# Optimization experiments

Hardware: AMD Instinct MI355X
Metric: run time of the kernel (lower is better)

## Reference

```python
import jax, jax.numpy as jnp
import numpy as np

PI = np.pi
B_IN, B1, B2 = 30, 10, 6      # bandwidths: input S2, after conv1, after conv2
F1, F2, F_OUT = 20, 40, 10


def _wigner_d_stack(l, betas):
    """Wigner-d d^l_{mn}(beta) = <m|exp(-i beta Jy)|n> (real), shape [nbeta, 2l+1, 2l+1]."""
    n = 2 * l + 1
    m = np.arange(-l, l)
    c = np.sqrt(l * (l + 1) - m * (m + 1))          # J+ couplings m -> m+1
    Jp = np.zeros((n, n))
    Jp[np.arange(1, n), np.arange(n - 1)] = c
    A = 0.5 * (Jp.T - Jp)                            # exp(beta*A) = d^l(beta)
    ev, V = np.linalg.eig(A)
    Vi = np.linalg.inv(V)
    E = np.exp(np.multiply.outer(np.asarray(betas, np.float64), ev))
    return np.einsum('mk,bk,kn->bmn', V, E, Vi).real


def _qw(b):
    """Driscoll-Healy quadrature weights over beta for the SOFT grid of bandwidth b."""
    j = np.arange(2 * b)
    theta = PI * (2 * j + 1) / (4 * b)
    k = np.arange(b)
    return (2.0 / b) * np.sin(theta) * (np.sin(theta[:, None] * (2 * k + 1)) / (2 * k + 1)).sum(1)


def _betas(b):
    return PI * (2 * np.arange(2 * b) + 1) / (4 * b)


def _s2_grid():   # s2_near_identity_grid(): 3 betas x 8 alphas = 24 points
    beta = np.arange(1, 4) * (PI / 8) / 3
    alpha = np.linspace(0, 2 * PI, 8, endpoint=False)
    B, A = np.meshgrid(beta, alpha, indexing='ij')
    return B.ravel(), A.ravel()


def _so3_grid():  # so3_near_identity_grid(): 3x8x8 = 192 points, gamma = pre_gamma - alpha
    beta = np.arange(1, 4) * (PI / 8) / 3
    alpha = np.linspace(0, 2 * PI, 8, endpoint=False)
    pre_gamma = np.linspace(-2 * PI, 2 * PI, 8, endpoint=False)
    B, A, C = np.meshgrid(beta, alpha, pre_gamma, indexing='ij')
    return B.ravel(), A.ravel(), (C - A).ravel()


# ---------- static spectral constants (numpy, built once at import) ----------
_bet_in, _w_in = _betas(B_IN), _qw(B_IN)
_bet1, _w1 = _betas(B1), _qw(B1)
_bet2, _w2 = _betas(B2), _qw(B2)
_gb, _ga = _s2_grid()
_gb3, _ga3, _gc3 = _so3_grid()

# conv1 analysis: w(beta) * d^l_{m0}(beta_in), flattened over (l,m), l < B1
_dm1, _mi1, _y1 = [], [], []
for l in range(B1):
    d = _wigner_d_stack(l, _bet_in)                        # [60, 2l+1, 2l+1]
    _dm1.append((d[:, :, l] * _w_in[:, None]).T)           # [2l+1, 60] (column n=0)
    m = np.arange(-l, l + 1)
    _mi1.append(m % (2 * B_IN))
    dg = _wigner_d_stack(l, _gb)[:, :, l]                  # [24, 2l+1]
    _y1.append(np.exp(-1j * np.outer(m, _ga)) * dg.T)      # kernel rft basis [2l+1, 24]
DM1 = np.concatenate(_dm1, 0).astype(np.float32)           # [100, 60]
MI1 = np.concatenate(_mi1, 0)
Y1B = np.concatenate(_y1, 0).astype(np.complex64)          # [100, 24]

D_B1 = [_wigner_d_stack(l, _bet1) for l in range(B1)]      # d^l at the 20 betas of b=10 grid

# conv2 analysis: w(beta) * d^l_{mn}(beta_1), flattened over (l,m,n), l < B2
_dm2, _mi2, _ni2, _y2 = [], [], [], []
for l in range(B2):
    m = np.arange(-l, l + 1)
    d = D_B1[l]                                            # [20, 2l+1, 2l+1]
    _dm2.append((d * _w1[:, None, None]).reshape(2 * B1, -1).T)   # [(2l+1)^2, 20]
    mm, nn = np.meshgrid(m, m, indexing='ij')
    _mi2.append(mm.ravel() % (2 * B1))
    _ni2.append(nn.ravel() % (2 * B1))
    dg = _wigner_d_stack(l, _gb3)                          # [192, 2l+1, 2l+1]
    ph = np.exp(-1j * (np.multiply.outer(m, _ga3)[:, None, :] +
                       np.multiply.outer(m, _gc3)[None, :, :]))   # [2l+1,2l+1,192]
    _y2.append((np.moveaxis(dg, 0, -1) * ph).reshape(-1, _gb3.size))
DM2 = np.concatenate(_dm2, 0).astype(np.float32)           # [286, 20]
MI2 = np.concatenate(_mi2, 0)
NI2 = np.concatenate(_ni2, 0)
Y2B = np.concatenate(_y2, 0).astype(np.complex64)          # [286, 192]

D_B1F = [d.astype(np.float32) for d in D_B1]
D_B2F = [_wigner_d_stack(l, _bet2).astype(np.float32) for l in range(B2)]

SC1 = np.float32(1.0 / np.sqrt(_gb.size * 1))    # kernel scalings (s2cnn-style init scale)
SC2 = np.float32(1.0 / np.sqrt(_gb3.size * F1))
W2J = _w2.astype(np.float32)
INTEG_SCALE = np.float32((2 * PI / (2 * B2)) ** 2)


def _forward(x, kernel1, kernel2, w_out, bias_out):
    Bt = x.shape[0]
    # ---- S2Convolution: S2-FFT(x), rft(kernel), s2_mm, SO3-iFFT ----
    xh = jnp.fft.fft(x, axis=-1) / (2 * B_IN)                     # [B,1,60,60] cplx (alpha FFT)
    xg = xh[..., jnp.asarray(MI1)]                                # [B,1,60,100]
    X = jnp.einsum('kj,bfjk->kbf', jnp.asarray(DM1), xg)          # [100,B,1] spectral F^l_m
    Yk = jnp.einsum('kg,iog->kio', jnp.asarray(Y1B), kernel1.astype(jnp.complex64)) * SC1
    S = jnp.zeros((Bt, F1, 2 * B1, 2 * B1, 2 * B1), jnp.complex64)
    off = 0
    for l in range(B1):
        L = 2 * l + 1
        Z = jnp.einsum('mbi,nio->mnbo', X[off:off + L], jnp.conj(Yk[off:off + L]))
        T = jnp.einsum('jmn,mnbo->bojmn', float(2 * l + 1) * jnp.asarray(D_B1F[l]), Z)
        mi = np.arange(-l, l + 1) % (2 * B1)
        S = S.at[:, :, :, mi[:, None], mi[None, :]].add(T)
        off += L
    x1 = jnp.fft.ifft2(S, axes=(-2, -1)).real * float((2 * B1) ** 2)   # [B,F1,20,20,20]
    x1 = jax.nn.relu(x1)
    # ---- SO3Convolution: SO3-FFT, rft(kernel), so3_mm, SO3-iFFT ----
    xh2 = jnp.fft.fft2(x1, axes=(-2, -1)) / float((2 * B1) ** 2)       # alpha,gamma FFT
    xg2 = xh2[:, :, :, jnp.asarray(MI2), jnp.asarray(NI2)]             # [B,F1,20,286]
    X2 = jnp.einsum('kj,bfjk->kbf', jnp.asarray(DM2), xg2)             # [286,B,F1]
    Yk2 = jnp.einsum('kg,iog->kio', jnp.asarray(Y2B), kernel2.astype(jnp.complex64)) * SC2
    S2 = jnp.zeros((Bt, F2, 2 * B2, 2 * B2, 2 * B2), jnp.complex64)
    off = 0
    for l in range(B2):
        L = 2 * l + 1
        X2l = X2[off:off + L * L].reshape(L, L, Bt, F1)     # [m,k,B,i]
        Y2l = Yk2[off:off + L * L].reshape(L, L, F1, F2)    # [n,k,i,o]
        Z = jnp.einsum('mkbi,nkio->mnbo', X2l, jnp.conj(Y2l))   # hat z^l = hat x^l hat y^l+
        T = jnp.einsum('jmn,mnbo->bojmn', float(2 * l + 1) * jnp.asarray(D_B2F[l]), Z)
        mi = np.arange(-l, l + 1) % (2 * B2)
        S2 = S2.at[:, :, :, mi[:, None], mi[None, :]].add(T)
        off += L * L
    x2 = jnp.fft.ifft2(S2, axes=(-2, -1)).real * float((2 * B2) ** 2)  # [B,F2,12,12,12]
    x2 = jax.nn.relu(x2)
    # ---- so3_integrate + linear head ----
    feat = INTEG_SCALE * jnp.einsum('bfjac,j->bf', x2, jnp.asarray(W2J))
    return feat @ w_out.T + bias_out


def setup_inputs() -> dict:
    key = jax.random.key(0)
    ks = jax.random.split(key, 5)
    return {
        'x': jax.random.normal(ks[0], (128, 1, 2 * B_IN, 2 * B_IN), jnp.float32),
        'kernel1': jax.random.normal(ks[1], (1, F1, 24), jnp.float32),
        'kernel2': jax.random.normal(ks[2], (F1, F2, 192), jnp.float32),
        'w_out': jax.random.normal(ks[3], (F_OUT, F2), jnp.float32) / np.sqrt(float(F2)),
        'bias_out': jax.random.normal(ks[4], (F_OUT,), jnp.float32) * 0.01,
    }


def reference(x, kernel1, kernel2, w_out, bias_out):
    return _forward(x, kernel1, kernel2, w_out, bias_out)
```

## Files before the change

### kernel.cpp

```cpp
#include <hip/hip_runtime.h>
#include <cmath>

#define NT 256
#define BT 128

#define OFF_W60   0
#define OFF_E20   2280
#define OFF_E12   2320
#define OFF_W2J   2344
#define OFF_DM1   2356
#define OFF_Y1B   8356
#define OFF_D1R   13156
#define OFF_DM2   39756
#define OFF_Y2B   45476
#define OFF_D2R   155300
#define OFF_T19U  158732
#define OFF_T11V  159492
#define OFF_T12U  159932
#define OFF_TABA  160196
#define OFF_TABB  161526
#define OFF_TH19  161812
#define OFF_TH12  162212
#define OFF_TABH  162356
#define OFF_TAH1  162504
#define OFF_DM2T  163220
#define OFF_TGIX  168940
#define OFF_QW30  169228
#define OFF_QW10  169288
#define OFF_QW6   169308
#define OFF_D3B   169320
#define OFF_PA    170178
#define OFF_PG    170354
#define OFF_END   171764
#define N_INIT1   1742
#define N_INIT2   109735

__constant__ int c_ZB1[10] = {0,1,10,35,84,165,286,455,680,969};
__constant__ int c_ZBH[10] = {0,1,7,22,50,95,161,252,372,525};
__constant__ int c_ZB2[6]  = {0,1,10,35,84,165};
__constant__ int c_BOFF[6] = {0,22,208,718,1712,3350};

__device__ inline void wsync() {
    __asm__ volatile("" ::: "memory");
    __builtin_amdgcn_s_waitcnt(0xC07F);
    __builtin_amdgcn_wave_barrier();
    __asm__ volatile("" ::: "memory");
}

__device__ inline double dipow(double x, int e) {
    double r = 1.0;
    for (int i = 0; i < e; ++i) r *= x;
    return r;
}

__device__ double wigd(const double* F, const double* Fi, int l, int mp, int m, double beta) {
    double cb = cos(beta * 0.5), sb = sin(beta * 0.5);
    int smin = m - mp; if (smin < 0) smin = 0;
    int smax = l + m;  if (l - mp < smax) smax = l - mp;
    double pref = sqrt(F[l+mp] * F[l-mp] * F[l+m] * F[l-m]);
    double sum = 0.0;
    for (int s = smin; s <= smax; ++s) {
        double t = pref * (Fi[l+m-s] * Fi[s] * Fi[mp-m+s] * Fi[l-mp-s]);
        t *= dipow(cb, 2*l + m - mp - 2*s) * dipow(sb, mp - m + 2*s);
        sum += ((mp - m + s) & 1) ? -t : t;
    }
    return sum;
}

__device__ double qwj(int bnd, int j) {
    const double PI = 3.14159265358979323846;
    double theta = PI * (2*j + 1) / (4.0 * bnd);
    double s = 0.0;
    for (int k = 0; k < bnd; ++k) s += sin(theta * (2*k + 1)) / (2*k + 1);
    return 2.0 / bnd * sin(theta) * s;
}

__global__ void k_init1(float* __restrict__ ws) {
    int idx = blockIdx.x * blockDim.x + threadIdx.x;
    if (idx >= N_INIT1) return;
    double F[20], Fi[20];
    F[0] = 1.0;
    #pragma unroll
    for (int i = 1; i < 20; ++i) F[i] = F[i-1] * i;
    Fi[19] = 1.0 / F[19];
    #pragma unroll
    for (int i = 18; i >= 0; --i) Fi[i] = Fi[i+1] * (i+1);
    const double PI = 3.14159265358979323846;

    if (idx < 60) {
        ws[OFF_QW30 + idx] = (float)qwj(30, idx);
    } else if (idx < 80) {
        ws[OFF_QW10 + idx - 60] = (float)qwj(10, idx - 60);
    } else if (idx < 92) {
        ws[OFF_QW6 + idx - 80] = (float)qwj(6, idx - 80);
    } else if (idx < 950) {
        int e = idx - 92; int k2 = e / 3, bi = e % 3;
        int l = 0; while (l < 5 && k2 >= c_ZB2[l+1]) ++l;
        int L = 2*l + 1, loc = k2 - c_ZB2[l];
        int m = loc / L - l, n = loc % L - l;
        double beta = (bi + 1) * (PI / 8.0) / 3.0;
        ws[OFF_D3B + e] = (float)wigd(F, Fi, l, m, n, beta);
    } else if (idx < 1038) {
        int e = idx - 950; int m = e / 8 - 5, ai = e % 8;
        double ph = -(double)m * (2.0 * PI * ai / 8.0);
        ws[OFF_PA + 2*e]     = (float)cos(ph);
        ws[OFF_PA + 2*e + 1] = (float)sin(ph);
    } else {
        int e = idx - 1038; int n = e / 64 - 5, g2 = e % 64, ai = g2 / 8, ci = g2 % 8;
        double alpha = 2.0 * PI * ai / 8.0;
        double gamma = (-2.0 * PI + ci * (PI / 2.0)) - alpha;
        double ph = -(double)n * gamma;
        ws[OFF_PG + 2*e]     = (float)cos(ph);
        ws[OFF_PG + 2*e + 1] = (float)sin(ph);
    }
}

__global__ void k_init2(float* __restrict__ ws) {
    int idx = blockIdx.x * blockDim.x + threadIdx.x;
    if (idx >= N_INIT2) return;
    double F[20], Fi[20];
    F[0] = 1.0;
    #pragma unroll
    for (int i = 1; i < 20; ++i) F[i] = F[i-1] * i;
    Fi[19] = 1.0 / F[19];
    #pragma unroll
    for (int i = 18; i >= 0; --i) Fi[i] = Fi[i+1] * (i+1);
    const double PI = 3.14159265358979323846;

    if (idx < 1140) {
        int r = idx / 60, a = idx % 60;
        double ang = -2.0 * PI * (double)((r - 9) * a) / 60.0;
        ws[OFF_W60 + 2*idx]     = (float)cos(ang);
        ws[OFF_W60 + 2*idx + 1] = (float)sin(ang);
    } else if (idx < 1160) {
        int t = idx - 1140;
        double ang = 2.0 * PI * t / 20.0;
        ws[OFF_E20 + 2*t]     = (float)cos(ang);
        ws[OFF_E20 + 2*t + 1] = (float)sin(ang);
    } else if (idx < 1172) {
        int t = idx - 1160;
        double ang = 2.0 * PI * t / 12.0;
        ws[OFF_E12 + 2*t]     = (float)cos(ang);
        ws[OFF_E12 + 2*t + 1] = (float)sin(ang);
    } else if (idx < 1184) {
        int j = idx - 1172;
        ws[OFF_W2J + j] = ws[OFF_QW6 + j];
    } else if (idx < 7184) {
        int e = idx - 1184; int k = e / 60, j = e % 60;
        int l = 0; while ((l + 1) * (l + 1) <= k) ++l;
        int m = k - l*l - l;
        double beta = PI * (2*j + 1) / 120.0;
        ws[OFF_DM1 + e] = (float)((double)ws[OFF_QW30 + j] * wigd(F, Fi, l, m, 0, beta));
    } else if (idx < 9584) {
        int e = idx - 7184; int k = e / 24, g = e % 24;
        int l = 0; while ((l + 1) * (l + 1) <= k) ++l;
        int m = k - l*l - l;
        int bi = g / 8, ai = g % 8;
        double beta  = (bi + 1) * (PI / 8.0) / 3.0;
        double alpha = 2.0 * PI * ai / 8.0;
        double d = wigd(F, Fi, l, m, 0, beta);
        double ph = -(double)m * alpha;
        ws[OFF_Y1B + 2*e]     = (float)(d * cos(ph));
        ws[OFF_Y1B + 2*e + 1] = (float)(d * sin(ph));
    } else if (idx < 36184) {
        int e = idx - 9584; int j = e / 1330, t = e % 1330;
        int l = 0; while (l < 9 && t >= c_ZB1[l+1]) ++l;
        int L = 2*l + 1, loc = t - c_ZB1[l];
        int mi = loc / L, ni = loc % L;
        double beta = PI * (2*j + 1) / 40.0;
        ws[OFF_D1R + e] = (float)((double)L * wigd(F, Fi, l, mi - l, ni - l, beta));
    } else if (idx < 41904) {
    } else if (idx < 96816) {
        int e = idx - 41904; int k2 = e / 192, g = e % 192;
        int l = 0; while (l < 5 && k2 >= c_ZB2[l+1]) ++l;
        int L = 2*l + 1, loc = k2 - c_ZB2[l];
        int m = loc / L - l, n = loc % L - l;
        int bi = g / 64, ai = (g / 8) % 8, ci = g % 8;
        float d = ws[OFF_D3B + k2 * 3 + bi];
        const float2 pa = ((const float2*)(ws + OFF_PA))[(m + 5) * 8 + ai];
        const float2 pg = ((const float2*)(ws + OFF_PG))[(n + 5) * 64 + ai * 8 + ci];
        ws[OFF_Y2B + 2*e]     = d * (pa.x * pg.x - pa.y * pg.y);
        ws[OFF_Y2B + 2*e + 1] = d * (pa.x * pg.y + pa.y * pg.x);
    } else if (idx < 100248) {
        int e = idx - 96816; int j = e / 286, t = e % 286;
        int l = 0; while (l < 5 && t >= c_ZB2[l+1]) ++l;
        int L = 2*l + 1, loc = t - c_ZB2[l];
        int mi = loc / L, ni = loc % L;
        double beta = PI * (2*j + 1) / 24.0;
        ws[OFF_D2R + e] = (float)((double)L * wigd(F, Fi, l, mi - l, ni - l, beta));
    } else if (idx < 100628) {
        int e = idx - 100248; int c = e / 19, n = e % 19 - 9;
        double ang = 2.0 * PI * (double)(n * c) / 20.0;
        ws[OFF_T19U + 2*e]     = (float)cos(ang);
        ws[OFF_T19U + 2*e + 1] = (float)sin(ang);
    } else if (idx < 100848) {
        int e = idx - 100628; int r = e / 20, c = e % 20;
        double ang = -2.0 * PI * (double)((r - 5) * c) / 20.0;
        ws[OFF_T11V + 2*e]     = (float)cos(ang);
        ws[OFF_T11V + 2*e + 1] = (float)sin(ang);
    } else if (idx < 100980) {
        int e = idx - 100848; int c = e / 11, n = e % 11 - 5;
        double ang = 2.0 * PI * (double)(n * c) / 12.0;
        ws[OFF_T12U + 2*e]     = (float)cos(ang);
        ws[OFF_T12U + 2*e + 1] = (float)sin(ang);
    } else if (idx < 102310) {
    } else if (idx < 102596) {
        int t = idx - 102310;
        int l = 0; while (l < 5 && t >= c_ZB2[l+1]) ++l;
        int L = 2*l + 1, loc = t - c_ZB2[l];
        ((int*)ws)[OFF_TABB + t] = l | ((loc / L) << 8) | ((loc % L) << 16);
    } else if (idx < 102796) {
        int e = idx - 102596; int a = e / 10, mm = e % 10;
        double f = (mm == 0) ? 1.0 : 2.0;
        double ang = 2.0 * PI * (double)(mm * a) / 20.0;
        ws[OFF_TH19 + 2*e]     = (float)(f * cos(ang));
        ws[OFF_TH19 + 2*e + 1] = (float)(f * sin(ang));
    } else if (idx < 102868) {
        int e = idx - 102796; int a = e / 6, mm = e % 6;
        double f = (mm == 0) ? 1.0 : 2.0;
        double ang = 2.0 * PI * (double)(mm * a) / 12.0;
        ws[OFF_TH12 + 2*e]     = (float)(f * cos(ang));
        ws[OFF_TH12 + 2*e + 1] = (float)(f * sin(ang));
    } else if (idx < 103014) {
        int t = idx - 102868;
        int l = 0, cum = 0, loc = 0;
        for (; l < 6; ++l) {
            int L = 2*l + 1, h = (L*L + 1) / 2;
            if (t < cum + h) { loc = t - cum; break; }
            cum += h;
        }
        ((int*)ws)[OFF_TABH + t] = l | (loc << 8);
    } else if (idx < 103729) {
        int t = idx - 103014;
        int l = 0; while (l < 9 && t >= c_ZBH[l+1]) ++l;
        int L = 2*l + 1, loc = t - c_ZBH[l];
        ((int*)ws)[OFF_TAH1 + t] = l | ((loc / L) << 8) | ((loc % L) << 16);
    } else if (idx < 109449) {
        int e = idx - 103729; int k2 = e / 20, j = e % 20;
        int l = 0; while (l < 5 && k2 >= c_ZB2[l+1]) ++l;
        int L = 2*l + 1, loc = k2 - c_ZB2[l];
        int mi = loc / L, ni = loc % L;
        double beta = PI * (2*j + 1) / 40.0;
        ws[OFF_DM2T + e] = (float)((double)ws[OFF_QW10 + j] *
                                   wigd(F, Fi, l, mi - l, ni - l, beta) / 400.0);
    } else {
        int t = idx - 109449;
        int l = 0; while (l < 5 && t >= c_ZB2[l+1]) ++l;
        int L = 2*l + 1, loc = t - c_ZB2[l];
        int m = loc / L - l, n = loc % L - l;
        int gi, sgbit;
        if (m >= 0) { gi = m * 11 + (n + 5); sgbit = 0; }
        else        { gi = (-m) * 11 + (5 - n); sgbit = 1; }
        ((int*)ws)[OFF_TGIX + t] = gi | (sgbit << 16);
    }
}

__global__ __launch_bounds__(NT) void k_front(
    const float* __restrict__ x, const float2* __restrict__ W60,
    const float* __restrict__ DM1, float2* __restrict__ X,
    const float* __restrict__ k1, const float2* __restrict__ Y1B,
    float2* __restrict__ Yk1) {
    const int bid = blockIdx.x;
    const int tid = threadIdx.x;
    if (bid < BT) {
        const int b = bid;
        __shared__ __align__(16) float  sx[3600];
        __shared__ __align__(16) float2 sW[1140];
        __shared__ __align__(16) float2 sxh[1140];
        for (int t = tid; t < 900; t += NT)
            ((float4*)sx)[t] = ((const float4*)(x + b * 3600))[t];
        for (int t = tid; t < 1140; t += NT) sW[t] = W60[t];
        __syncthreads();
        for (int t = tid; t < 1140; t += NT) {
            int r = t % 19, j = t / 19;
            const float* xr = sx + j * 60;
            const float2* wr = sW + r * 60;
            float re = 0.f, im = 0.f;
            for (int a = 0; a < 60; ++a) {
                float v = xr[a];
                float2 w = wr[a];
                re += v * w.x; im += v * w.y;
            }
            sxh[j * 19 + r] = make_float2(re * (1.f / 60.f), im * (1.f / 60.f));
        }
        __syncthreads();
        for (int k = tid; k < 100; k += NT) {
            int l = 0; while ((l + 1) * (l + 1) <= k) ++l;
            int r = (k - l*l - l) + 9;
            float re = 0.f, im = 0.f;
            for (int j = 0; j < 60; ++j) {
                float d = DM1[k * 60 + j];
                float2 v = sxh[j * 19 + r];
                re += d * v.x; im += d * v.y;
            }
            X[k * BT + b] = make_float2(re, im);
        }
    } else {
        int idx = (bid - BT) * NT + tid;
        if (idx >= 100 * 20) return;
        int o = idx % 20, k = idx / 20;
        float re = 0.f, im = 0.f;
        for (int g = 0; g < 24; ++g) {
            float2 y = Y1B[k * 24 + g];
            float w = k1[o * 24 + g];
            re += y.x * w; im += y.y * w;
        }
        const float SC1 = 0.20412414523193154f;
        Yk1[idx] = make_float2(re * SC1, im * SC1);
    }
}

__global__ __launch_bounds__(NT) void k_Yk2(const float* __restrict__ k2in,
                                            const float2* __restrict__ Y2B,
                                            const int* __restrict__ gTABH,
                                            float2* __restrict__ Yk2) {
    const int h = blockIdx.x >> 1;
    const int half = blockIdx.x & 1;
    const int tid = threadIdx.x;
    int ph = gTABH[h];
    int l = ph & 255, loc = ph >> 8;
    int L = 2 * l + 1;
    int mi = loc / L, ni = loc % L;
    int k2  = c_ZB2[l] + loc;
    int locm = L * L - 1 - loc;
    int k2m = c_ZB2[l] + locm;
    float par = ((mi + ni) & 1) ? -1.f : 1.f;

    __shared__ __align__(16) float2 sY[192];
    for (int t = tid; t < 192; t += NT) sY[t] = Y2B[k2 * 192 + t];
    __syncthreads();
    const float4* sY4 = (const float4*)sY;
    const float SC2 = 0.016137430609197573f;
    for (int t = half * 400 + tid; t < half * 400 + 400; t += NT) {
        int o = t / 20, i = t % 20;
        const float4* kp = (const float4*)(k2in + (i * 40 + o) * 192);
        float re = 0.f, im = 0.f;
        #pragma unroll 4
        for (int p = 0; p < 48; ++p) {
            float4 w = kp[p];
            float4 y01 = sY4[2*p], y23 = sY4[2*p + 1];
            re += w.x * y01.x + w.y * y01.z + w.z * y23.x + w.w * y23.z;
            im += w.x * y01.y + w.y * y01.w + w.z * y23.y + w.w * y23.w;
        }
        re *= SC2; im *= SC2;
        Yk2[(o * 286 + k2) * 20 + i] = make_float2(re, im);
        if (k2m != k2)
            Yk2[(o * 286 + k2m) * 20 + i] = make_float2(par * re, -par * im);
    }
}

__global__ __launch_bounds__(NT) void k_stage1(
    const float2* __restrict__ X, const float2* __restrict__ Yk1,
    const float* __restrict__ gD1R,
    const float2* __restrict__ gT19, const float2* __restrict__ gT11,
    const float2* __restrict__ gTH19,
    const int* __restrict__ gTAH1, const float* __restrict__ gDM2T,
    const int* __restrict__ gTGIX, float2* __restrict__ X2g) {
    const int b = blockIdx.x % BT;
    const int f = blockIdx.x / BT;
    const int tid = threadIdx.x;
    const int wv = tid >> 6, lane = tid & 63;

    __shared__ __align__(16) float2 sZ[715];
    __shared__ __align__(16) float2 sT19[440];
    __shared__ __align__(16) float2 sTH19[280];
    __shared__ __align__(16) float2 sT11[220];
    __shared__ __align__(16) float2 sGall[1320];
    __shared__ __align__(16) float2 sA[4][224];
    __shared__ __align__(16) float2 sB[4][280];

    for (int t = tid; t < 380; t += NT) sT19[(t / 19) * 22 + (t % 19)] = gT19[t];
    for (int t = tid; t < 200; t += NT) sTH19[(t / 10) * 14 + (t % 10)] = gTH19[t];
    for (int t = tid; t < 220; t += NT) sT11[t] = gT11[t];
    for (int t = tid; t < 715; t += NT) {
        int p = gTAH1[t];
        int l = p & 255, mm = (p >> 8) & 255, ni = p >> 16;
        float2 a = X[(l*l + l + mm) * BT + b];
        float2 y = Yk1[(l*l + ni) * 20 + f];
        sZ[t] = make_float2(a.x * y.x + a.y * y.y, a.y * y.x - a.x * y.y);
    }
    __syncthreads();

    float2* S   = sA[wv];
    float2* U   = sB[wv];
    float*  x1  = (float*)sA[wv];
    float2* V   = sB[wv];

    for (int jj = 0; jj < 5; ++jj) {
        const int j = wv + 4 * jj;

        {
            const float* dp = gD1R + j * 1330;
            for (int t = lane; t < 190; t += 64) {
                int mm = t / 19, ni = t % 19;
                int n = ni - 9;
                int an = n < 0 ? -n : n;
                int lmin = mm > an ? mm : an;
                float re = 0.f, im = 0.f;
                for (int l = lmin; l < 10; ++l) {
                    int L = 2*l + 1;
                    float dv = dp[c_ZB1[l] + (mm + l) * L + (n + l)];
                    float2 z = sZ[c_ZBH[l] + mm * L + (n + l)];
                    re += dv * z.x; im += dv * z.y;
                }
                S[mm * 22 + ni] = make_float2(re, im);
            }
        }
        wsync();

        for (int t = lane; t < 100; t += 64) {
            int mm = t / 10, c = t % 10;
            const float4* sp = (const float4*)(S + mm * 22);
            const float4* tp = (const float4*)(sT19 + c * 22);
            float re_e = 0.f, im_e = 0.f, re_o = 0.f, im_o = 0.f;
            #pragma unroll
            for (int p = 0; p < 9; ++p) {
                float4 s = sp[p], w = tp[p];
                re_o += s.x * w.x - s.y * w.y;  im_o += s.x * w.y + s.y * w.x;
                re_e += s.z * w.z - s.w * w.w;  im_e += s.z * w.w + s.w * w.z;
            }
            {
                float2 s1 = S[mm * 22 + 18], w1 = sT19[c * 22 + 18];
                re_o += s1.x * w1.x - s1.y * w1.y;
                im_o += s1.x * w1.y + s1.y * w1.x;
            }
            U[c * 14 + mm]        = make_float2(re_e + re_o, im_e + im_o);
            U[(c + 10) * 14 + mm] = make_float2(re_e - re_o, im_e - im_o);
        }
        wsync();

        for (int t = lane; t < 100; t += 64) {
            int cp = t % 10, ap = t / 10;
            const float4* u0 = (const float4*)(U + cp * 14);
            const float4* u1 = (const float4*)(U + (cp + 10) * 14);
            const float4* tp = (const float4*)(sTH19 + ap * 14);
            float e0 = 0.f, o0 = 0.f, e1 = 0.f, o1 = 0.f;
            #pragma unroll
            for (int p = 0; p < 5; ++p) {
                float4 w = tp[p];
                float4 ua = u0[p], ub = u1[p];
                e0 += ua.x * w.x - ua.y * w.y;
                o0 += ua.z * w.z - ua.w * w.w;
                e1 += ub.x * w.x - ub.y * w.y;
                o1 += ub.z * w.z - ub.w * w.w;
            }
            float v;
            v = e0 + o0; x1[ap * 20 + cp]             = v > 0.f ? v : 0.f;
            v = e0 - o0; x1[(ap + 10) * 20 + cp]      = v > 0.f ? v : 0.f;
            v = e1 + o1; x1[ap * 20 + cp + 10]        = v > 0.f ? v : 0.f;
            v = e1 - o1; x1[(ap + 10) * 20 + cp + 10] = v > 0.f ? v : 0.f;
        }
        wsync();

        for (int t = lane; t < 120; t += 64) {
            int nn = t / 20, a = t % 20;
            const float4* xp = (const float4*)(x1 + a * 20);
            const float4* tp = (const float4*)(sT11 + (nn + 5) * 20);
            float r0 = 0.f, i0 = 0.f, r1 = 0.f, i1 = 0.f;
            #pragma unroll
            for (int p = 0; p < 5; ++p) {
                float4 xv = xp[p];
                float4 t01 = tp[2*p], t23 = tp[2*p + 1];
                r0 += xv.x * t01.x + xv.y * t01.z;
                i0 += xv.x * t01.y + xv.y * t01.w;
                r1 += xv.z * t23.x + xv.w * t23.z;
                i1 += xv.z * t23.y + xv.w * t23.w;
            }
            V[nn * 22 + a] = make_float2(r0 + r1, i0 + i1);
        }
        wsync();

        for (int t = lane; t < 66; t += 64) {
            int mm = t / 11, ni2 = t % 11;
            int nn2 = ni2 - 5;
            int na = nn2 < 0 ? -nn2 : nn2;
            float s = nn2 < 0 ? -1.f : 1.f;
            const float4* vp = (const float4*)(V + na * 22);
            const float4* tp = (const float4*)(sT11 + (mm + 5) * 20);
            float r0 = 0.f, i0 = 0.f, r1 = 0.f, i1 = 0.f;
            #pragma unroll
            for (int q = 0; q < 10; ++q) {
                float4 v = vp[q], w = tp[q];
                float vy0 = s * v.y, vy1 = s * v.w;
                r0 += v.x * w.x - vy0 * w.y;
                i0 += v.x * w.y + vy0 * w.x;
                r1 += v.z * w.z - vy1 * w.w;
                i1 += v.z * w.w + vy1 * w.z;
            }
            sGall[j * 66 + t] = make_float2(r0 + r1, i0 + i1);
        }
        wsync();
    }
    __syncthreads();

    for (int k2 = tid; k2 < 286; k2 += NT) {
        int e = gTGIX[k2];
        int gi = e & 0xFFFF;
        float sg = (e >> 16) ? -1.f : 1.f;
        const float* dm = gDM2T + k2 * 20;
        float re = 0.f, im = 0.f;
        #pragma unroll
        for (int j = 0; j < 20; ++j) {
            float d = dm[j];
            float2 g = sGall[j * 66 + gi];
            re += d * g.x; im += d * g.y;
        }
        X2g[b * 5720 + k2 * 20 + f] = make_float2(re, sg * im);
    }
}

__global__ __launch_bounds__(NT) void k_Z2(
    const float2* __restrict__ X2g, const float2* __restrict__ Yk2,
    const int* __restrict__ gTABB, const int* __restrict__ gTABH,
    float2* __restrict__ Z2g) {
    const int bt   = blockIdx.x & 15;
    const int part = (blockIdx.x >> 4) & 1;
    const int o    = blockIdx.x >> 5;
    const int b0 = bt * 8;
    const int tid = threadIdx.x;

    __shared__ __align__(16) float2 sB[3350];

    const int sub  = part ? 3350 : 0;
    const int stN  = part ? 2420 : 3300;
    const int k2b  = part ? 165 : 0;
    const float2* Bg = Yk2 + o * 5720 + k2b * 20;
    for (int e = tid; e < stN; e += NT) {
        int k2 = k2b + e / 20, i = e % 20;
        int p = gTABB[k2];
        int l = p & 255, r = (p >> 8) & 255, kk = p >> 16;
        sB[c_BOFF[l] - sub + r * (40 * l + 22) + kk * 20 + i] = Bg[e];
    }
    __syncthreads();

    const int perb  = part ? 61 : 85;
    const int hbase = part ? 85 : 0;
    for (int q = tid; q < 8 * perb; q += NT) {
        int b_local = q / perb, h = hbase + q % perb;
        int ph = gTABH[h];
        int l = ph & 255, loc = ph >> 8;
        int L = 2 * l + 1;
        int mi = loc / L, ni = loc % L;
        const float4* ap = (const float4*)(X2g + (size_t)(b0 + b_local) * 5720
                                           + (c_ZB2[l] + mi * L) * 20);
        const float4* bp = (const float4*)(sB + c_BOFF[l] - sub + ni * (40 * l + 22));
        float re = 0.f, im = 0.f;
        int n4 = 10 * L;
        for (int p4 = 0; p4 < n4; ++p4) {
            float4 a = ap[p4], y = bp[p4];
            re += a.x * y.x + a.y * y.y + a.z * y.z + a.w * y.w;
            im += a.y * y.x - a.x * y.y + a.w * y.z - a.z * y.w;
        }
        size_t base = ((size_t)(b0 + b_local) * 40 + o) * 286;
        Z2g[base + c_ZB2[l] + loc] = make_float2(re, im);
        int locm = L * L - 1 - loc;
        if (locm != loc) {
            float sg = ((mi + ni) & 1) ? -1.f : 1.f;
            Z2g[base + c_ZB2[l] + locm] = make_float2(sg * re, -sg * im);
        }
    }
}

__global__ __launch_bounds__(128) void k_stage2b(
    const float2* __restrict__ Z2g, const float* __restrict__ gD2R,
    const float2* __restrict__ gT12, const float2* __restrict__ gTH12,
    const float* __restrict__ gW2J, float* __restrict__ feat) {
    const int b = blockIdx.x % BT;
    const int o = blockIdx.x / BT;
    const int tid = threadIdx.x;
    const int wv = tid >> 6, lane = tid & 63;

    __shared__ __align__(16) float2 sZb[286];
    __shared__ __align__(16) float2 sT12[168];
    __shared__ __align__(16) float2 sTH12[96];
    __shared__ __align__(16) float2 sS[2][88];
    __shared__ __align__(16) float2 sU[2][96];
    __shared__ float sredw[2];

    const float2* Zr = Z2g + ((size_t)b * 40 + o) * 286;
    for (int t = tid; t < 286; t += 128) sZb[t] = Zr[t];
    for (int t = tid; t < 132; t += 128) sT12[(t / 11) * 14 + (t % 11)] = gT12[t];
    for (int t = tid; t < 72; t += 128) sTH12[(t / 6) * 8 + (t % 6)] = gTH12[t];
    __syncthreads();

    float2* S = sS[wv];
    float2* U = sU[wv];
    float facc = 0.f;

    for (int jj = 0; jj < 6; ++jj) {
        const int j = wv + 2 * jj;

        {
            const float* dp = gD2R + j * 286;
            for (int t = lane; t < 66; t += 64) {
                int mm = t / 11, ni = t % 11;
                int n = ni - 5;
                int an = n < 0 ? -n : n;
                int lmin = mm > an ? mm : an;
                float re = 0.f, im = 0.f;
                for (int l = lmin; l < 6; ++l) {
                    int L = 2*l + 1;
                    int off = c_ZB2[l] + (mm + l) * L + (n + l);
                    float dv = dp[off];
                    float2 z = sZb[off];
                    re += dv * z.x; im += dv * z.y;
                }
                S[mm * 14 + ni] = make_float2(re, im);
            }
        }
        wsync();

        for (int t = lane; t < 72; t += 64) {
            int mm = t / 12, c = t % 12;
            const float4* sp = (const float4*)(S + mm * 14);
            const float4* tp = (const float4*)(sT12 + c * 14);
            float re = 0.f, im = 0.f;
            #pragma unroll
            for (int p = 0; p < 5; ++p) {
                float4 s = sp[p], w = tp[p];
                re += s.x * w.x - s.y * w.y + s.z * w.z - s.w * w.w;
                im += s.x * w.y + s.y * w.x + s.z * w.w + s.w * w.z;
            }
            float2 s1 = S[mm * 14 + 10], w1 = sT12[c * 14 + 10];
            re += s1.x * w1.x - s1.y * w1.y;
            im += s1.x * w1.y + s1.y * w1.x;
            U[c * 8 + mm] = make_float2(re, im);
        }
        wsync();

        {
            float wj = gW2J[j];
            for (int t = lane; t < 144; t += 64) {
                int a = t / 12, c = t % 12;
                const float4* up = (const float4*)(U + c * 8);
                const float4* tp = (const float4*)(sTH12 + a * 8);
                float acc = 0.f;
                #pragma unroll
                for (int p = 0; p < 3; ++p) {
                    float4 u = up[p], w = tp[p];
                    acc += u.x * w.x - u.y * w.y + u.z * w.z - u.w * w.w;
                }
                if (acc > 0.f) facc += wj * acc;
            }
        }
        wsync();
    }

    #pragma unroll
    for (int d = 32; d > 0; d >>= 1) facc += __shfl_down(facc, d, 64);
    if (lane == 0) sredw[wv] = facc;
    __syncthreads();
    if (tid == 0) {
        const float INTEG = 0.27415567780803774f;
        feat[b * 40 + o] = (sredw[0] + sredw[1]) * INTEG;
    }
}

__global__ void k_out(const float* __restrict__ feat, const float* __restrict__ w,
                      const float* __restrict__ bias, float* __restrict__ out) {
    int idx = blockIdx.x * blockDim.x + threadIdx.x;
    if (idx >= BT * 10) return;
    int fo = idx % 10, b = idx / 10;
    float acc = bias[fo];
    for (int o2 = 0; o2 < 40; ++o2) acc += feat[b * 40 + o2] * w[fo * 40 + o2];
    out[idx] = acc;
}

extern "C" void kernel_launch(void* const* d_in, const int* in_sizes, int n_in,
                              void* d_out, int out_size, void* d_ws, size_t ws_size,
                              hipStream_t stream) {
    (void)in_sizes; (void)n_in; (void)out_size; (void)ws_size;
    const float* x   = (const float*)d_in[0];
    const float* k1  = (const float*)d_in[1];
    const float* k2  = (const float*)d_in[2];
    const float* wO  = (const float*)d_in[3];
    const float* bO  = (const float*)d_in[4];
    float* out = (float*)d_out;

    float* ws = (float*)d_ws;
    const float2* cW60 = (const float2*)(ws + OFF_W60);
    const float*  cW2J = ws + OFF_W2J;
    const float*  cDM1 = ws + OFF_DM1;
    const float2* cY1B = (const float2*)(ws + OFF_Y1B);
    const float*  gD1R = ws + OFF_D1R;
    const float2* cY2B = (const float2*)(ws + OFF_Y2B);
    const float*  gD2R = ws + OFF_D2R;
    const float2* gT19 = (const float2*)(ws + OFF_T19U);
    const float2* gT11 = (const float2*)(ws + OFF_T11V);
    const float2* gT12 = (const float2*)(ws + OFF_T12U);
    const float2* gTH19 = (const float2*)(ws + OFF_TH19);
    const float2* gTH12 = (const float2*)(ws + OFF_TH12);
    const int*    gTABB = (const int*)(ws + OFF_TABB);
    const int*    gTABH = (const int*)(ws + OFF_TABH);
    const int*    gTAH1 = (const int*)(ws + OFF_TAH1);
    const float*  gDM2T = ws + OFF_DM2T;
    const int*    gTGIX = (const int*)(ws + OFF_TGIX);

    float2* X    = (float2*)(ws + OFF_END);
    float2* Yk1  = X + 100 * BT;
    float2* Yk2  = Yk1 + 100 * 20;
    float2* X2   = Yk2 + 40 * 286 * 20;
    float*  feat = (float*)(X2 + (size_t)BT * 5720);
    float2* Z2   = (float2*)(feat + BT * 40);

    k_init1<<<(N_INIT1 + NT - 1) / NT, NT, 0, stream>>>(ws);
    k_init2<<<(N_INIT2 + NT - 1) / NT, NT, 0, stream>>>(ws);
    k_front<<<BT + 8, NT, 0, stream>>>(x, cW60, cDM1, X, k1, cY1B, Yk1);
    k_Yk2<<<292, NT, 0, stream>>>(k2, cY2B, gTABH, Yk2);
    k_stage1<<<BT * 20, NT, 0, stream>>>(X, Yk1, gD1R, gT19, gT11, gTH19, gTAH1,
                                         gDM2T, gTGIX, X2);
    k_Z2<<<1280, NT, 0, stream>>>(X2, Yk2, gTABB, gTABH, Z2);
    k_stage2b<<<BT * 40, 128, 0, stream>>>(Z2, gD2R, gT12, gTH12, cW2J, feat);
    k_out<<<(BT * 10 + NT - 1) / NT, NT, 0, stream>>>(feat, wO, bO, out);
}
```

Measured before the change: 363.6 us.

## Fuse Z2 spectral product into stage-2 inverse transform kernel

Merges k_Z2 and k_stage2b into one kernel, k_s2. Each block stages the full Yk2 slice for one output channel in shared memory, computes the Z2 coefficients for 8 batch items straight into shared memory, and then runs the inverse SO(3) transform, ReLU and integration using 4 waves. This removes the Z2 global round trip and one launch. In exchange the grid drops to 640 blocks and shared memory per block grows to about 50KB, which lowers occupancy. The Z2 phase also uses only 146 of 256 threads per batch item.

```diff
diff --git a/kernel.cpp b/kernel.cpp
--- a/kernel.cpp
+++ b/kernel.cpp
@@ -509,150 +509,136 @@
     }
 }
 
-__global__ __launch_bounds__(NT) void k_Z2(
+__global__ __launch_bounds__(NT) void k_s2(
     const float2* __restrict__ X2g, const float2* __restrict__ Yk2,
     const int* __restrict__ gTABB, const int* __restrict__ gTABH,
-    float2* __restrict__ Z2g) {
-    const int bt   = blockIdx.x & 15;
-    const int part = (blockIdx.x >> 4) & 1;
-    const int o    = blockIdx.x >> 5;
+    const float* __restrict__ gD2R, const float2* __restrict__ gT12,
+    const float2* __restrict__ gTH12, const float* __restrict__ gW2J,
+    float* __restrict__ feat) {
+    const int bt = blockIdx.x & 15;
+    const int o  = blockIdx.x >> 4;
     const int b0 = bt * 8;
     const int tid = threadIdx.x;
-
-    __shared__ __align__(16) float2 sB[3350];
-
-    const int sub  = part ? 3350 : 0;
-    const int stN  = part ? 2420 : 3300;
-    const int k2b  = part ? 165 : 0;
-    const float2* Bg = Yk2 + o * 5720 + k2b * 20;
-    for (int e = tid; e < stN; e += NT) {
-        int k2 = k2b + e / 20, i = e % 20;
-        int p = gTABB[k2];
-        int l = p & 255, r = (p >> 8) & 255, kk = p >> 16;
-        sB[c_BOFF[l] - sub + r * (40 * l + 22) + kk * 20 + i] = Bg[e];
-    }
-    __syncthreads();
-
-    const int perb  = part ? 61 : 85;
-    const int hbase = part ? 85 : 0;
-    for (int q = tid; q < 8 * perb; q += NT) {
-        int b_local = q / perb, h = hbase + q % perb;
-        int ph = gTABH[h];
-        int l = ph & 255, loc = ph >> 8;
-        int L = 2 * l + 1;
-        int mi = loc / L, ni = loc % L;
-        const float4* ap = (const float4*)(X2g + (size_t)(b0 + b_local) * 5720
-                                           + (c_ZB2[l] + mi * L) * 20);
-        const float4* bp = (const float4*)(sB + c_BOFF[l] - sub + ni * (40 * l + 22));
-        float re = 0.f, im = 0.f;
-        int n4 = 10 * L;
-        for (int p4 = 0; p4 < n4; ++p4) {
-            float4 a = ap[p4], y = bp[p4];
-            re += a.x * y.x + a.y * y.y + a.z * y.z + a.w * y.w;
-            im += a.y * y.x - a.x * y.y + a.w * y.z - a.z * y.w;
-        }
-        size_t base = ((size_t)(b0 + b_local) * 40 + o) * 286;
-        Z2g[base + c_ZB2[l] + loc] = make_float2(re, im);
-        int locm = L * L - 1 - loc;
-        if (locm != loc) {
-            float sg = ((mi + ni) & 1) ? -1.f : 1.f;
-            Z2g[base + c_ZB2[l] + locm] = make_float2(sg * re, -sg * im);
-        }
-    }
-}
-
-__global__ __launch_bounds__(128) void k_stage2b(
-    const float2* __restrict__ Z2g, const float* __restrict__ gD2R,
-    const float2* __restrict__ gT12, const float2* __restrict__ gTH12,
-    const float* __restrict__ gW2J, float* __restrict__ feat) {
-    const int b = blockIdx.x % BT;
-    const int o = blockIdx.x / BT;
-    const int tid = threadIdx.x;
     const int wv = tid >> 6, lane = tid & 63;
 
+    __shared__ __align__(16) float2 sB[5792];
     __shared__ __align__(16) float2 sZb[286];
     __shared__ __align__(16) float2 sT12[168];
     __shared__ __align__(16) float2 sTH12[96];
-    __shared__ __align__(16) float2 sS[2][88];
-    __shared__ __align__(16) float2 sU[2][96];
-    __shared__ float sredw[2];
-
-    const float2* Zr = Z2g + ((size_t)b * 40 + o) * 286;
-    for (int t = tid; t < 286; t += 128) sZb[t] = Zr[t];
-    for (int t = tid; t < 132; t += 128) sT12[(t / 11) * 14 + (t % 11)] = gT12[t];
-    for (int t = tid; t < 72; t += 128) sTH12[(t / 6) * 8 + (t % 6)] = gTH12[t];
+    __shared__ __align__(16) float2 sS[4][88];
+    __shared__ __align__(16) float2 sU[4][96];
+    __shared__ float sredw[4];
+
+    const float2* Bg = Yk2 + o * 5720;
+    for (int e = tid; e < 5720; e += NT) {
+        int k2 = e / 20, i = e % 20;
+        int p = gTABB[k2];
+        int l = p & 255, r = (p >> 8) & 255, kk = p >> 16;
+        sB[c_BOFF[l] + r * (40 * l + 22) + kk * 20 + i] = Bg[e];
+    }
+    for (int t = tid; t < 132; t += NT) sT12[(t / 11) * 14 + (t % 11)] = gT12[t];
+    for (int t = tid; t < 72; t += NT) sTH12[(t / 6) * 8 + (t % 6)] = gTH12[t];
     __syncthreads();
 
     float2* S = sS[wv];
     float2* U = sU[wv];
-    float facc = 0.f;
-
-    for (int jj = 0; jj < 6; ++jj) {
-        const int j = wv + 2 * jj;
-
-        {
-            const float* dp = gD2R + j * 286;
-            for (int t = lane; t < 66; t += 64) {
-                int mm = t / 11, ni = t % 11;
-                int n = ni - 5;
-                int an = n < 0 ? -n : n;
-                int lmin = mm > an ? mm : an;
+
+    for (int bl = 0; bl < 8; ++bl) {
+        const int b = b0 + bl;
+
+        for (int h = tid; h < 146; h += NT) {
+            int ph = gTABH[h];
+            int l = ph & 255, loc = ph >> 8;
+            int L = 2 * l + 1;
+            int mi = loc / L, ni = loc % L;
+            const float4* ap = (const float4*)(X2g + (size_t)b * 5720
+                                               + (c_ZB2[l] + mi * L) * 20);
+            const float4* bp = (const float4*)(sB + c_BOFF[l] + ni * (40 * l + 22));
+            float re = 0.f, im = 0.f;
+            int n4 = 10 * L;
+            for (int p4 = 0; p4 < n4; ++p4) {
+                float4 a = ap[p4], y = bp[p4];
+                re += a.x * y.x + a.y * y.y + a.z * y.z + a.w * y.w;
+                im += a.y * y.x - a.x * y.y + a.w * y.z - a.z * y.w;
+            }
+            sZb[c_ZB2[l] + loc] = make_float2(re, im);
+            int locm = L * L - 1 - loc;
+            if (locm != loc) {
+                float sg = ((mi + ni) & 1) ? -1.f : 1.f;
+                sZb[c_ZB2[l] + locm] = make_float2(sg * re, -sg * im);
+            }
+        }
+        __syncthreads();
+
+        float facc = 0.f;
+        for (int jj = 0; jj < 3; ++jj) {
+            const int j = wv + 4 * jj;
+
+            {
+                const float* dp = gD2R + j * 286;
+                for (int t = lane; t < 66; t += 64) {
+                    int mm = t / 11, ni = t % 11;
+                    int n = ni - 5;
+                    int an = n < 0 ? -n : n;
+                    int lmin = mm > an ? mm : an;
+                    float re = 0.f, im = 0.f;
+                    for (int l = lmin; l < 6; ++l) {
+                        int L = 2*l + 1;
+                        int off = c_ZB2[l] + (mm + l) * L + (n + l);
+                        float dv = dp[off];
+                        float2 z = sZb[off];
+                        re += dv * z.x; im += dv * z.y;
+                    }
+                    S[mm * 14 + ni] = make_float2(re, im);
+                }
+            }
+            wsync();
+
+            for (int t = lane; t < 72; t += 64) {
+                int mm = t / 12, c = t % 12;
+                const float4* sp = (const float4*)(S + mm * 14);
+                const float4* tp = (const float4*)(sT12 + c * 14);
                 float re = 0.f, im = 0.f;
-                for (int l = lmin; l < 6; ++l) {
-                    int L = 2*l + 1;
-                    int off = c_ZB2[l] + (mm + l) * L + (n + l);
-                    float dv = dp[off];
-                    float2 z = sZb[off];
-                    re += dv * z.x; im += dv * z.y;
+                #pragma unroll
+                for (int p = 0; p < 5; ++p) {
+                    float4 s = sp[p], w = tp[p];
+                    re += s.x * w.x - s.y * w.y + s.z * w.z - s.w * w.w;
+                    im += s.x * w.y + s.y * w.x + s.z * w.w + s.w * w.z;
                 }
-                S[mm * 14 + ni] = make_float2(re, im);
-            }
-        }
-        wsync();
-
-        for (int t = lane; t < 72; t += 64) {
-            int mm = t / 12, c = t % 12;
-            const float4* sp = (const float4*)(S + mm * 14);
-            const float4* tp = (const float4*)(sT12 + c * 14);
-            float re = 0.f, im = 0.f;
-            #pragma unroll
-            for (int p = 0; p < 5; ++p) {
-                float4 s = sp[p], w = tp[p];
-                re += s.x * w.x - s.y * w.y + s.z * w.z - s.w * w.w;
-                im += s.x * w.y + s.y * w.x + s.z * w.w + s.w * w.z;
-            }
-            float2 s1 = S[mm * 14 + 10], w1 = sT12[c * 14 + 10];
-            re += s1.x * w1.x - s1.y * w1.y;
-            im += s1.x * w1.y + s1.y * w1.x;
-            U[c * 8 + mm] = make_float2(re, im);
-        }
-        wsync();
-
-        {
-            float wj = gW2J[j];
-            for (int t = lane; t < 144; t += 64) {
-                int a = t / 12, c = t % 12;
-                const float4* up = (const float4*)(U + c * 8);
-                const float4* tp = (const float4*)(sTH12 + a * 8);
-                float acc = 0.f;
-                #pragma unroll
-                for (int p = 0; p < 3; ++p) {
-                    float4 u = up[p], w = tp[p];
-                    acc += u.x * w.x - u.y * w.y + u.z * w.z - u.w * w.w;
+                float2 s1 = S[mm * 14 + 10], w1 = sT12[c * 14 + 10];
+                re += s1.x * w1.x - s1.y * w1.y;
+                im += s1.x * w1.y + s1.y * w1.x;
+                U[c * 8 + mm] = make_float2(re, im);
+            }
+            wsync();
+
+            {
+                float wj = gW2J[j];
+                for (int t = lane; t < 144; t += 64) {
+                    int a = t / 12, c = t % 12;
+                    const float4* up = (const float4*)(U + c * 8);
+                    const float4* tp = (const float4*)(sTH12 + a * 8);
+                    float acc = 0.f;
+                    #pragma unroll
+                    for (int p = 0; p < 3; ++p) {
+                        float4 u = up[p], w = tp[p];
+                        acc += u.x * w.x - u.y * w.y + u.z * w.z - u.w * w.w;
+                    }
+                    if (acc > 0.f) facc += wj * acc;
                 }
-                if (acc > 0.f) facc += wj * acc;
-            }
-        }
-        wsync();
-    }
-
-    #pragma unroll
-    for (int d = 32; d > 0; d >>= 1) facc += __shfl_down(facc, d, 64);
-    if (lane == 0) sredw[wv] = facc;
-    __syncthreads();
-    if (tid == 0) {
-        const float INTEG = 0.27415567780803774f;
-        feat[b * 40 + o] = (sredw[0] + sredw[1]) * INTEG;
+            }
+            wsync();
+        }
+
+        #pragma unroll
+        for (int d = 32; d > 0; d >>= 1) facc += __shfl_down(facc, d, 64);
+        if (lane == 0) sredw[wv] = facc;
+        __syncthreads();
+        if (tid == 0) {
+            const float INTEG = 0.27415567780803774f;
+            feat[b * 40 + o] = (sredw[0] + sredw[1] + sredw[2] + sredw[3]) * INTEG;
+        }
+        __syncthreads();
     }
 }
 
@@ -701,7 +687,6 @@
     float2* Yk2  = Yk1 + 100 * 20;
     float2* X2   = Yk2 + 40 * 286 * 20;
     float*  feat = (float*)(X2 + (size_t)BT * 5720);
-    float2* Z2   = (float2*)(feat + BT * 40);
 
     k_init1<<<(N_INIT1 + NT - 1) / NT, NT, 0, stream>>>(ws);
     k_init2<<<(N_INIT2 + NT - 1) / NT, NT, 0, stream>>>(ws);
@@ -709,7 +694,6 @@
     k_Yk2<<<292, NT, 0, stream>>>(k2, cY2B, gTABH, Yk2);
     k_stage1<<<BT * 20, NT, 0, stream>>>(X, Yk1, gD1R, gT19, gT11, gTH19, gTAH1,
                                          gDM2T, gTGIX, X2);
-    k_Z2<<<1280, NT, 0, stream>>>(X2, Yk2, gTABB, gTABH, Z2);
-    k_stage2b<<<BT * 40, 128, 0, stream>>>(Z2, gD2R, gT12, gTH12, cW2J, feat);
+    k_s2<<<640, NT, 0, stream>>>(X2, Yk2, gTABB, gTABH, gD2R, gT12, gTH12, cW2J, feat);
     k_out<<<(BT * 10 + NT - 1) / NT, NT, 0, stream>>>(feat, wO, bO, out);
 }
```

Measured after the change: 510.9 us. 40.5% more time.
